# Performance work log

Hardware: AMD Instinct MI355X
Metric: run time of the kernel (lower is better)

The kernel has to match this reference:

```python
import jax, jax.numpy as jnp
import numpy as np

B, T, H, C_CLS = 1024, 256, 256, 10
SIGMA = 1.0 / H


def setup_inputs() -> dict:
    key = jax.random.key(0)
    ks = jax.random.split(key, 10)
    n = lambda k, shp: SIGMA * jax.random.normal(k, shp, dtype=jnp.float32)
    return {
        "x": jax.random.normal(ks[0], (B, T), dtype=jnp.float32),
        "W_gx": n(ks[1], (1, H)), "W_gh": n(ks[2], (H, H)), "b_g": jnp.zeros(H, jnp.float32),
        "W_ix": n(ks[3], (1, H)), "W_ih": n(ks[4], (H, H)), "b_i": jnp.zeros(H, jnp.float32),
        "W_fx": n(ks[5], (1, H)), "W_fh": n(ks[6], (H, H)), "b_f": jnp.zeros(H, jnp.float32),
        "W_ox": n(ks[7], (1, H)), "W_oh": n(ks[8], (H, H)), "b_o": jnp.zeros(H, jnp.float32),
        "W_ph": n(ks[9], (H, C_CLS)), "b_p": jnp.zeros(C_CLS, jnp.float32),
    }


def reference(x, W_gx, W_gh, b_g, W_ix, W_ih, b_i, W_fx, W_fh, b_f, W_ox, W_oh, b_o, W_ph, b_p):
    batch = x.shape[0]
    hdim = W_gh.shape[0]

    def step(carry, x_t):
        h, c = carry
        xi = x_t[:, None]  # [B,1] scalar input per step
        g = jnp.tanh(xi @ W_gx + h @ W_gh + b_g)
        i = jax.nn.sigmoid(xi @ W_ix + h @ W_ih + b_i)
        # NOTE: original torch code swaps b_o/b_f in f_t/o_t; preserved faithfully.
        f = jax.nn.sigmoid(xi @ W_fx + h @ W_fh + b_o)
        o = jax.nn.sigmoid(xi @ W_ox + h @ W_oh + b_f)
        c = g * i + c * f
        h = jnp.tanh(c) * o
        return (h, c), None

    h0 = jnp.zeros((batch, hdim), x.dtype)
    c0 = jnp.zeros((batch, hdim), x.dtype)
    (h_T, _), _ = jax.lax.scan(step, (h0, c0), x.T)  # scan over time [T,B]
    # original computes p_t every step but only returns the last one
    return h_T @ W_ph + b_p
```

## Files before the change

kernel.cpp:

```cpp
#include <hip/hip_runtime.h>


#define Bsz   1024
#define Tt    256
#define Hh    256
#define NCLS  10
#define NTHR  512
#define HSZ64 ((size_t)Bsz * Hh)

typedef float f32x4 __attribute__((ext_vector_type(4)));
typedef short s16x8 __attribute__((ext_vector_type(8)));
typedef unsigned int u32;
typedef unsigned long long u64;

#define HOWNB  32768
#define SMEMB  (32768 + 2 * 576 * 4)

__device__ __forceinline__ unsigned short f2bf(float f) {
    u32 u = __builtin_bit_cast(u32, f);
    return (unsigned short)((u + 0x7FFFu + ((u >> 16) & 1u)) >> 16);
}
__device__ __forceinline__ float bf2f(unsigned short b) {
    u32 u = ((u32)b) << 16;
    return __builtin_bit_cast(float, u);
}
template<int CTRL>
__device__ __forceinline__ float quadf(float v) {
    return __builtin_bit_cast(float,
        __builtin_amdgcn_update_dpp(0, __builtin_bit_cast(int, v),
                                    CTRL, 0xF, 0xF, true));
}
__device__ __forceinline__ float fast_tanh(float v) {
    const float e = __expf(-2.0f * fabsf(v));
    const float t = (1.0f - e) * __builtin_amdgcn_rcpf(1.0f + e);
    return copysignf(t, v);
}
__device__ __forceinline__ u64 coh_load64(const u64* p) {
    return __hip_atomic_load((u64*)p, __ATOMIC_RELAXED, __HIP_MEMORY_SCOPE_AGENT);
}
__device__ __forceinline__ void coh_store64(u64* p, u64 v) {
    __hip_atomic_store(p, v, __ATOMIC_RELAXED, __HIP_MEMORY_SCOPE_AGENT);
}

extern "C" __global__ void __launch_bounds__(NTHR, 2)
lstm_v14(const float* __restrict__ x,
         const float* __restrict__ W_gx, const float* __restrict__ W_gh, const float* __restrict__ b_g,
         const float* __restrict__ W_ix, const float* __restrict__ W_ih, const float* __restrict__ b_i,
         const float* __restrict__ W_fx, const float* __restrict__ W_fh, const float* __restrict__ b_f,
         const float* __restrict__ W_ox, const float* __restrict__ W_oh, const float* __restrict__ b_o,
         const float* __restrict__ W_ph, const float* __restrict__ b_p,
         float* __restrict__ out, u64* __restrict__ hx)
{
    __shared__ __align__(16) char smem[SMEMB];
    u32* hown = (u32*)(smem + HOWNB);

    const int tid  = threadIdx.x;
    const int lane = tid & 63;
    const int wv   = tid >> 6;
    const int br   = blockIdx.x & 31;
    const int cg   = blockIdx.x >> 5;
    const int r0   = br * 32;

    const int gate   = lane & 3;
    const int hcol_l = wv * 4 + ((lane & 15) >> 2);
    const int hcol_g = cg * 32 + hcol_l;
    const int krow   = lane >> 4;

    const float* __restrict__ Wg =
        (gate == 0) ? W_gh : (gate == 1) ? W_ih : (gate == 2) ? W_fh : W_oh;
    s16x8 bw1[8], bw2[8];
    #pragma unroll
    for (int ks = 0; ks < 8; ++ks) {
        s16x8 v1, v2;
        #pragma unroll
        for (int e = 0; e < 8; ++e) {
            const float w = Wg[(size_t)(ks * 32 + krow * 8 + e) * Hh + hcol_g];
            const unsigned short c1 = f2bf(w);
            const unsigned short c2 = f2bf(w - bf2f(c1));
            v1[e] = (short)c1; v2[e] = (short)c2;
        }
        bw1[ks] = v1; bw2[ks] = v2;
    }

    const float wx = ((gate == 0) ? W_gx : (gate == 1) ? W_ix : (gate == 2) ? W_fx : W_ox)[hcol_g];
    const float bb = ((gate == 0) ? b_g  : (gate == 1) ? b_i  : (gate == 2) ? b_o  : b_f )[hcol_g];
    float cA[4], cB[4];
    #pragma unroll
    for (int r = 0; r < 4; ++r) { cA[r] = 0.0f; cB[r] = 0.0f; }

    const int sr = lane >> 2;
    const int c8 = (lane & 3) * 8;

    for (int i = tid; i < 2 * 576; i += NTHR) hown[i] = 0u;
    __syncthreads();

    auto substep = [&](int t, int ch, float* cst) {
        u32 packed[8];
        if (wv != cg) {
            const u64* src = hx + (size_t)(t & 1) * HSZ64
                           + (size_t)(r0 + ch * 16 + sr) * Hh + wv * 32 + c8;
            u64 q[8];
            for (;;) {
                #pragma unroll
                for (int i = 0; i < 8; ++i) q[i] = coh_load64(src + i);
                bool ok = true;
                #pragma unroll
                for (int i = 0; i < 8; ++i) ok = ok && ((u32)(q[i] >> 32) == (u32)t);
                if (__all(ok)) break;
                __builtin_amdgcn_s_sleep(1);
            }
            #pragma unroll
            for (int i = 0; i < 8; ++i) packed[i] = (u32)q[i];
        } else {
            const u32* hp = hown + ch * 576 + sr * 36 + c8;
            const uint4 q0 = *(const uint4*)hp;
            const uint4 q1 = *(const uint4*)(hp + 4);
            packed[0] = q0.x; packed[1] = q0.y; packed[2] = q0.z; packed[3] = q0.w;
            packed[4] = q1.x; packed[5] = q1.y; packed[6] = q1.z; packed[7] = q1.w;
        }
        {
            u32 lo[4], hi[4];
            #pragma unroll
            for (int i = 0; i < 4; ++i) {
                const u32 p0 = packed[2 * i], p1 = packed[2 * i + 1];
                lo[i] = (p0 & 0xffffu) | (p1 << 16);
                hi[i] = (p0 >> 16)     | (p1 & 0xffff0000u);
            }
            char* pb = smem + ch * 16384 + wv * 1024 + ((((lane & 3) << 4) + sr) << 4);
            *(uint4*)pb          = *(uint4*)lo;
            *(uint4*)(pb + 8192) = *(uint4*)hi;
        }
        __syncthreads();

        f32x4 aA = {0.f,0.f,0.f,0.f}, aB = {0.f,0.f,0.f,0.f}, aC = {0.f,0.f,0.f,0.f};
        #pragma unroll
        for (int ks = 0; ks < 8; ++ks) {
            const char* ab = smem + ch * 16384 + ks * 1024 + lane * 16;
            const s16x8 a1 = *(const s16x8*)ab;
            const s16x8 a2 = *(const s16x8*)(ab + 8192);
            aA = __builtin_amdgcn_mfma_f32_16x16x32_bf16(a1, bw1[ks], aA, 0, 0, 0);
            aB = __builtin_amdgcn_mfma_f32_16x16x32_bf16(a2, bw1[ks], aB, 0, 0, 0);
            aC = __builtin_amdgcn_mfma_f32_16x16x32_bf16(a1, bw2[ks], aC, 0, 0, 0);
        }
        const f32x4 acc = aA + aB + aC;

        #pragma unroll
        for (int r = 0; r < 4; ++r) {
            const int rowl = krow * 4 + r;
            const int row  = ch * 16 + rowl;
            const float xval = x[(size_t)(r0 + row) * Tt + t];
            const float pre  = acc[r] + fmaf(xval, wx, bb);
            const float vin  = (gate == 0) ? 2.0f * pre : pre;
            const float e    = __expf(-fabsf(vin));
            const float rc   = __builtin_amdgcn_rcpf(1.0f + e);
            const float sig  = (vin >= 0.0f) ? rc : 1.0f - rc;
            const float th   = copysignf((1.0f - e) * rc, pre);
            const float act  = (gate == 0) ? th : sig;
            const float gv = quadf<0x00>(act);
            const float iv = quadf<0x55>(act);
            const float fv = quadf<0xAA>(act);
            const float ov = quadf<0xFF>(act);
            cst[r] = fmaf(gv, iv, cst[r] * fv);
            const float hv = fast_tanh(cst[r]) * ov;
            if (gate == 0) {
                const unsigned short h1 = f2bf(hv);
                const unsigned short h2 = f2bf(hv - bf2f(h1));
                const u32 pk = (u32)h1 | ((u32)h2 << 16);
                coh_store64(hx + (size_t)((t + 1) & 1) * HSZ64
                               + (size_t)(r0 + row) * Hh + hcol_g,
                            ((u64)(u32)(t + 1) << 32) | (u64)pk);
                hown[ch * 576 + rowl * 36 + hcol_l] = pk;
            }
        }
    };

    for (int t = 0; t < Tt; ++t) {
        substep(t, 0, cA);
        substep(t, 1, cB);
    }

    if (cg == 0) {
        __syncthreads();
        u32* tile = (u32*)smem;
        const u64* src = hx + (size_t)r0 * Hh;
        for (int i = tid; i < 32 * Hh; i += NTHR) {
            u64 q = coh_load64(src + i);
            while ((u32)(q >> 32) != (u32)Tt) {
                __builtin_amdgcn_s_sleep(1);
                q = coh_load64(src + i);
            }
            tile[i] = (u32)q;
        }
        __syncthreads();
        for (int idx = tid; idx < 32 * NCLS; idx += NTHR) {
            const int row = idx / NCLS;
            const int cc  = idx - row * NCLS;
            float a = b_p[cc];
            for (int k = 0; k < Hh; ++k) {
                const u32 p = tile[row * Hh + k];
                a = fmaf(bf2f((unsigned short)p) + bf2f((unsigned short)(p >> 16)),
                         W_ph[k * NCLS + cc], a);
            }
            out[(size_t)(r0 + row) * NCLS + cc] = a;
        }
    }
}

extern "C" void kernel_launch(void* const* d_in, const int* in_sizes, int n_in,
                              void* d_out, int out_size, void* d_ws, size_t ws_size,
                              hipStream_t stream) {
    const float* x    = (const float*)d_in[0];
    const float* W_gx = (const float*)d_in[1];
    const float* W_gh = (const float*)d_in[2];
    const float* b_g  = (const float*)d_in[3];
    const float* W_ix = (const float*)d_in[4];
    const float* W_ih = (const float*)d_in[5];
    const float* b_i  = (const float*)d_in[6];
    const float* W_fx = (const float*)d_in[7];
    const float* W_fh = (const float*)d_in[8];
    const float* b_f  = (const float*)d_in[9];
    const float* W_ox = (const float*)d_in[10];
    const float* W_oh = (const float*)d_in[11];
    const float* b_o  = (const float*)d_in[12];
    const float* W_ph = (const float*)d_in[13];
    const float* b_p  = (const float*)d_in[14];
    float* out = (float*)d_out;

    u64* hx = (u64*)d_ws;
    const size_t clear_bytes = 2 * HSZ64 * sizeof(u64);

    hipMemsetAsync(d_ws, 0, clear_bytes, stream);

    lstm_v14<<<dim3(256), dim3(NTHR), 0, stream>>>(
        x, W_gx, W_gh, b_g, W_ix, W_ih, b_i, W_fx, W_fh, b_f,
        W_ox, W_oh, b_o, W_ph, b_p, out, hx);
}
```

Before: 1.989 ms.

## Replace persistent spin-wait kernel with per-timestep kernel launches

Replaces the persistent kernel, which synchronised blocks through flag-tagged global h stores and spin polling, with one kernel launch per timestep. h and c state now live in global workspace buffers, and stream ordering replaces the inter-block flags. A prep kernel converts the recurrent weights to split-bf16 fragments once, and a separate head kernel computes the output projection. This removes spin-wait and coherent-load overhead but adds 256 launch overheads and a reload of weights and cell state on every step.

```diff
diff --git a/kernel.cpp b/kernel.cpp
--- a/kernel.cpp
+++ b/kernel.cpp
@@ -6,15 +6,11 @@
 #define Hh    256
 #define NCLS  10
 #define NTHR  512
-#define HSZ64 ((size_t)Bsz * Hh)
+#define WSPN  32768
 
 typedef float f32x4 __attribute__((ext_vector_type(4)));
 typedef short s16x8 __attribute__((ext_vector_type(8)));
 typedef unsigned int u32;
-typedef unsigned long long u64;
-
-#define HOWNB  32768
-#define SMEMB  (32768 + 2 * 576 * 4)
 
 __device__ __forceinline__ unsigned short f2bf(float f) {
     u32 u = __builtin_bit_cast(u32, f);
@@ -35,107 +31,103 @@
     const float t = (1.0f - e) * __builtin_amdgcn_rcpf(1.0f + e);
     return copysignf(t, v);
 }
-__device__ __forceinline__ u64 coh_load64(const u64* p) {
-    return __hip_atomic_load((u64*)p, __ATOMIC_RELAXED, __HIP_MEMORY_SCOPE_AGENT);
-}
-__device__ __forceinline__ void coh_store64(u64* p, u64 v) {
-    __hip_atomic_store(p, v, __ATOMIC_RELAXED, __HIP_MEMORY_SCOPE_AGENT);
+
+extern "C" __global__ void __launch_bounds__(256)
+lstm_prep(const float* __restrict__ W_gh, const float* __restrict__ W_ih,
+          const float* __restrict__ W_fh, const float* __restrict__ W_oh,
+          short* __restrict__ wsp)
+{
+    const int idx  = blockIdx.x * 256 + threadIdx.x;
+    const int lane = idx & 63;
+    const int ks   = (idx >> 6) & 7;
+    const int wv   = (idx >> 9) & 7;
+    const int cg   = idx >> 12;
+    const int gate = lane & 3;
+    const int hcol_g = cg * 32 + wv * 4 + ((lane & 15) >> 2);
+    const int krow = lane >> 4;
+    const float* __restrict__ Wg =
+        (gate == 0) ? W_gh : (gate == 1) ? W_ih : (gate == 2) ? W_fh : W_oh;
+    s16x8 v1, v2;
+    #pragma unroll
+    for (int e = 0; e < 8; ++e) {
+        const float w = Wg[(size_t)(ks * 32 + krow * 8 + e) * Hh + hcol_g];
+        const unsigned short c1 = f2bf(w);
+        const unsigned short c2 = f2bf(w - bf2f(c1));
+        v1[e] = (short)c1; v2[e] = (short)c2;
+    }
+    *(s16x8*)(wsp + (size_t)idx * 8)          = v1;
+    *(s16x8*)(wsp + (size_t)(WSPN + idx) * 8) = v2;
 }
 
 extern "C" __global__ void __launch_bounds__(NTHR, 2)
-lstm_v14(const float* __restrict__ x,
-         const float* __restrict__ W_gx, const float* __restrict__ W_gh, const float* __restrict__ b_g,
-         const float* __restrict__ W_ix, const float* __restrict__ W_ih, const float* __restrict__ b_i,
-         const float* __restrict__ W_fx, const float* __restrict__ W_fh, const float* __restrict__ b_f,
-         const float* __restrict__ W_ox, const float* __restrict__ W_oh, const float* __restrict__ b_o,
-         const float* __restrict__ W_ph, const float* __restrict__ b_p,
-         float* __restrict__ out, u64* __restrict__ hx)
+lstm_step(const float* __restrict__ x,
+          const float* __restrict__ W_gx, const float* __restrict__ b_g,
+          const float* __restrict__ W_ix, const float* __restrict__ b_i,
+          const float* __restrict__ W_fx, const float* __restrict__ b_f,
+          const float* __restrict__ W_ox, const float* __restrict__ b_o,
+          const short* __restrict__ wsp,
+          const u32* __restrict__ hcur, u32* __restrict__ hnxt,
+          float* __restrict__ cst, int t)
 {
-    __shared__ __align__(16) char smem[SMEMB];
-    u32* hown = (u32*)(smem + HOWNB);
+    __shared__ __align__(16) char smem[32768];
 
     const int tid  = threadIdx.x;
     const int lane = tid & 63;
     const int wv   = tid >> 6;
-    const int br   = blockIdx.x & 31;
-    const int cg   = blockIdx.x >> 5;
-    const int r0   = br * 32;
+    const int cg   = blockIdx.x & 7;
+    const int rg   = blockIdx.x >> 3;
+    const int r0   = rg * 32;
 
     const int gate   = lane & 3;
-    const int hcol_l = wv * 4 + ((lane & 15) >> 2);
-    const int hcol_g = cg * 32 + hcol_l;
+    const int hcol_g = cg * 32 + wv * 4 + ((lane & 15) >> 2);
     const int krow   = lane >> 4;
 
-    const float* __restrict__ Wg =
-        (gate == 0) ? W_gh : (gate == 1) ? W_ih : (gate == 2) ? W_fh : W_oh;
+    const s16x8* __restrict__ W1 =
+        (const s16x8*)wsp + ((size_t)(cg * 8 + wv) * 8 * 64 + lane);
     s16x8 bw1[8], bw2[8];
     #pragma unroll
     for (int ks = 0; ks < 8; ++ks) {
-        s16x8 v1, v2;
-        #pragma unroll
-        for (int e = 0; e < 8; ++e) {
-            const float w = Wg[(size_t)(ks * 32 + krow * 8 + e) * Hh + hcol_g];
-            const unsigned short c1 = f2bf(w);
-            const unsigned short c2 = f2bf(w - bf2f(c1));
-            v1[e] = (short)c1; v2[e] = (short)c2;
-        }
-        bw1[ks] = v1; bw2[ks] = v2;
+        bw1[ks] = W1[ks * 64];
+        bw2[ks] = W1[WSPN + ks * 64];
     }
 
     const float wx = ((gate == 0) ? W_gx : (gate == 1) ? W_ix : (gate == 2) ? W_fx : W_ox)[hcol_g];
     const float bb = ((gate == 0) ? b_g  : (gate == 1) ? b_i  : (gate == 2) ? b_o  : b_f )[hcol_g];
-    float cA[4], cB[4];
-    #pragma unroll
-    for (int r = 0; r < 4; ++r) { cA[r] = 0.0f; cB[r] = 0.0f; }
-
-    const int sr = lane >> 2;
-    const int c8 = (lane & 3) * 8;
-
-    for (int i = tid; i < 2 * 576; i += NTHR) hown[i] = 0u;
+
+    float cold[2][4], xv[2][4];
+    #pragma unroll
+    for (int half = 0; half < 2; ++half)
+        #pragma unroll
+        for (int r = 0; r < 4; ++r) {
+            const int row = r0 + half * 16 + krow * 4 + r;
+            cold[half][r] = cst[(size_t)row * Hh + hcol_g];
+            xv[half][r]   = x[(size_t)row * Tt + t];
+        }
+
+    const int sr = lane & 15;
+    const int c8 = (lane >> 4) * 8;
+    #pragma unroll
+    for (int half = 0; half < 2; ++half) {
+        const u32* src = hcur + (size_t)(r0 + half * 16 + sr) * Hh + wv * 32 + c8;
+        const uint4 a = *(const uint4*)src;
+        const uint4 b = *(const uint4*)(src + 4);
+        u32 lo[4], hi[4];
+        lo[0] = (a.x & 0xffffu) | (a.y << 16);  hi[0] = (a.x >> 16) | (a.y & 0xffff0000u);
+        lo[1] = (a.z & 0xffffu) | (a.w << 16);  hi[1] = (a.z >> 16) | (a.w & 0xffff0000u);
+        lo[2] = (b.x & 0xffffu) | (b.y << 16);  hi[2] = (b.x >> 16) | (b.y & 0xffff0000u);
+        lo[3] = (b.z & 0xffffu) | (b.w << 16);  hi[3] = (b.z >> 16) | (b.w & 0xffff0000u);
+        char* pb = smem + half * 16384 + wv * 1024 + lane * 16;
+        *(uint4*)pb          = *(uint4*)lo;
+        *(uint4*)(pb + 8192) = *(uint4*)hi;
+    }
     __syncthreads();
 
-    auto substep = [&](int t, int ch, float* cst) {
-        u32 packed[8];
-        if (wv != cg) {
-            const u64* src = hx + (size_t)(t & 1) * HSZ64
-                           + (size_t)(r0 + ch * 16 + sr) * Hh + wv * 32 + c8;
-            u64 q[8];
-            for (;;) {
-                #pragma unroll
-                for (int i = 0; i < 8; ++i) q[i] = coh_load64(src + i);
-                bool ok = true;
-                #pragma unroll
-                for (int i = 0; i < 8; ++i) ok = ok && ((u32)(q[i] >> 32) == (u32)t);
-                if (__all(ok)) break;
-                __builtin_amdgcn_s_sleep(1);
-            }
-            #pragma unroll
-            for (int i = 0; i < 8; ++i) packed[i] = (u32)q[i];
-        } else {
-            const u32* hp = hown + ch * 576 + sr * 36 + c8;
-            const uint4 q0 = *(const uint4*)hp;
-            const uint4 q1 = *(const uint4*)(hp + 4);
-            packed[0] = q0.x; packed[1] = q0.y; packed[2] = q0.z; packed[3] = q0.w;
-            packed[4] = q1.x; packed[5] = q1.y; packed[6] = q1.z; packed[7] = q1.w;
-        }
-        {
-            u32 lo[4], hi[4];
-            #pragma unroll
-            for (int i = 0; i < 4; ++i) {
-                const u32 p0 = packed[2 * i], p1 = packed[2 * i + 1];
-                lo[i] = (p0 & 0xffffu) | (p1 << 16);
-                hi[i] = (p0 >> 16)     | (p1 & 0xffff0000u);
-            }
-            char* pb = smem + ch * 16384 + wv * 1024 + ((((lane & 3) << 4) + sr) << 4);
-            *(uint4*)pb          = *(uint4*)lo;
-            *(uint4*)(pb + 8192) = *(uint4*)hi;
-        }
-        __syncthreads();
-
+    #pragma unroll
+    for (int half = 0; half < 2; ++half) {
         f32x4 aA = {0.f,0.f,0.f,0.f}, aB = {0.f,0.f,0.f,0.f}, aC = {0.f,0.f,0.f,0.f};
         #pragma unroll
         for (int ks = 0; ks < 8; ++ks) {
-            const char* ab = smem + ch * 16384 + ks * 1024 + lane * 16;
+            const char* ab = smem + half * 16384 + ks * 1024 + lane * 16;
             const s16x8 a1 = *(const s16x8*)ab;
             const s16x8 a2 = *(const s16x8*)(ab + 8192);
             aA = __builtin_amdgcn_mfma_f32_16x16x32_bf16(a1, bw1[ks], aA, 0, 0, 0);
@@ -146,63 +138,50 @@
 
         #pragma unroll
         for (int r = 0; r < 4; ++r) {
-            const int rowl = krow * 4 + r;
-            const int row  = ch * 16 + rowl;
-            const float xval = x[(size_t)(r0 + row) * Tt + t];
-            const float pre  = acc[r] + fmaf(xval, wx, bb);
-            const float vin  = (gate == 0) ? 2.0f * pre : pre;
-            const float e    = __expf(-fabsf(vin));
-            const float rc   = __builtin_amdgcn_rcpf(1.0f + e);
-            const float sig  = (vin >= 0.0f) ? rc : 1.0f - rc;
-            const float th   = copysignf((1.0f - e) * rc, pre);
-            const float act  = (gate == 0) ? th : sig;
+            const int row = r0 + half * 16 + krow * 4 + r;
+            const float pre = acc[r] + fmaf(xv[half][r], wx, bb);
+            const float vin = (gate == 0) ? 2.0f * pre : pre;
+            const float e   = __expf(-fabsf(vin));
+            const float rc  = __builtin_amdgcn_rcpf(1.0f + e);
+            const float sig = (vin >= 0.0f) ? rc : 1.0f - rc;
+            const float th  = copysignf((1.0f - e) * rc, pre);
+            const float act = (gate == 0) ? th : sig;
             const float gv = quadf<0x00>(act);
             const float iv = quadf<0x55>(act);
             const float fv = quadf<0xAA>(act);
             const float ov = quadf<0xFF>(act);
-            cst[r] = fmaf(gv, iv, cst[r] * fv);
-            const float hv = fast_tanh(cst[r]) * ov;
+            const float cnew = fmaf(gv, iv, cold[half][r] * fv);
+            const float hv   = fast_tanh(cnew) * ov;
             if (gate == 0) {
+                cst[(size_t)row * Hh + hcol_g] = cnew;
                 const unsigned short h1 = f2bf(hv);
                 const unsigned short h2 = f2bf(hv - bf2f(h1));
-                const u32 pk = (u32)h1 | ((u32)h2 << 16);
-                coh_store64(hx + (size_t)((t + 1) & 1) * HSZ64
-                               + (size_t)(r0 + row) * Hh + hcol_g,
-                            ((u64)(u32)(t + 1) << 32) | (u64)pk);
-                hown[ch * 576 + rowl * 36 + hcol_l] = pk;
+                hnxt[(size_t)row * Hh + hcol_g] = (u32)h1 | ((u32)h2 << 16);
             }
         }
-    };
-
-    for (int t = 0; t < Tt; ++t) {
-        substep(t, 0, cA);
-        substep(t, 1, cB);
-    }
-
-    if (cg == 0) {
-        __syncthreads();
-        u32* tile = (u32*)smem;
-        const u64* src = hx + (size_t)r0 * Hh;
-        for (int i = tid; i < 32 * Hh; i += NTHR) {
-            u64 q = coh_load64(src + i);
-            while ((u32)(q >> 32) != (u32)Tt) {
-                __builtin_amdgcn_s_sleep(1);
-                q = coh_load64(src + i);
-            }
-            tile[i] = (u32)q;
-        }
-        __syncthreads();
-        for (int idx = tid; idx < 32 * NCLS; idx += NTHR) {
-            const int row = idx / NCLS;
-            const int cc  = idx - row * NCLS;
-            float a = b_p[cc];
-            for (int k = 0; k < Hh; ++k) {
-                const u32 p = tile[row * Hh + k];
-                a = fmaf(bf2f((unsigned short)p) + bf2f((unsigned short)(p >> 16)),
-                         W_ph[k * NCLS + cc], a);
-            }
-            out[(size_t)(r0 + row) * NCLS + cc] = a;
-        }
+    }
+}
+
+extern "C" __global__ void __launch_bounds__(256)
+lstm_head(const u32* __restrict__ hT, const float* __restrict__ W_ph,
+          const float* __restrict__ b_p, float* __restrict__ out)
+{
+    __shared__ u32 tile[32 * Hh];
+    const int tid = threadIdx.x;
+    const int r0  = blockIdx.x * 32;
+    for (int i = tid; i < 32 * Hh; i += 256)
+        tile[i] = hT[(size_t)r0 * Hh + i];
+    __syncthreads();
+    for (int idx = tid; idx < 32 * NCLS; idx += 256) {
+        const int row = idx / NCLS;
+        const int cc  = idx - row * NCLS;
+        float a = b_p[cc];
+        for (int k = 0; k < Hh; ++k) {
+            const u32 p = tile[row * Hh + k];
+            a = fmaf(bf2f((unsigned short)p) + bf2f((unsigned short)(p >> 16)),
+                     W_ph[k * NCLS + cc], a);
+        }
+        out[(size_t)(r0 + row) * NCLS + cc] = a;
     }
 }
 
@@ -226,12 +205,22 @@
     const float* b_p  = (const float*)d_in[14];
     float* out = (float*)d_out;
 
-    u64* hx = (u64*)d_ws;
-    const size_t clear_bytes = 2 * HSZ64 * sizeof(u64);
-
-    hipMemsetAsync(d_ws, 0, clear_bytes, stream);
-
-    lstm_v14<<<dim3(256), dim3(NTHR), 0, stream>>>(
-        x, W_gx, W_gh, b_g, W_ix, W_ih, b_i, W_fx, W_fh, b_f,
-        W_ox, W_oh, b_o, W_ph, b_p, out, hx);
-}
+    u32*   hbuf0 = (u32*)d_ws;
+    u32*   hbuf1 = (u32*)((char*)d_ws + (1u << 20));
+    float* cst   = (float*)((char*)d_ws + (2u << 20));
+    short* wsp   = (short*)((char*)d_ws + (3u << 20));
+
+    hipMemsetAsync(d_ws, 0, 3u << 20, stream);
+
+    lstm_prep<<<dim3(128), dim3(256), 0, stream>>>(W_gh, W_ih, W_fh, W_oh, wsp);
+
+    for (int t = 0; t < Tt; ++t) {
+        const u32* hcur = (t & 1) ? hbuf1 : hbuf0;
+        u32*       hnxt = (t & 1) ? hbuf0 : hbuf1;
+        lstm_step<<<dim3(256), dim3(NTHR), 0, stream>>>(
+            x, W_gx, b_g, W_ix, b_i, W_fx, b_f, W_ox, b_o,
+            wsp, hcur, hnxt, cst, t);
+    }
+
+    lstm_head<<<dim3(32), dim3(256), 0, stream>>>(hbuf0, W_ph, b_p, out);
+}
```

Result: faster. 1.752 ms (-11.9%).
